# Kernel optimization log

Hardware: AMD Instinct MI355X
Metric: run time of the kernel (lower is better)

Reference implementation:

```python
import jax, jax.numpy as jnp
import numpy as np
from jax import lax

B, H, W, N = 4, 256, 256, 200000
DN = ('NHWC', 'HWIO', 'NHWC')


def _conv(x, w, padding):
    return lax.conv_general_dilated(x, w, (1, 1), padding, dimension_numbers=DN)


def _convT(x, w):
    # ConvTranspose2d(k=3, stride=2, padding=0): out = 2*H + 1
    return lax.conv_transpose(x, w, (2, 2), 'VALID', dimension_numbers=DN)


def setup_inputs() -> dict:
    key = jax.random.key(0)
    ks = jax.random.split(key, 12)
    features = jax.random.normal(ks[0], (N, 32), jnp.float32)
    bi = jax.random.randint(ks[1], (N, 1), 0, B)
    yi = jax.random.randint(ks[2], (N, 1), 0, H)
    xi = jax.random.randint(ks[3], (N, 1), 0, W)
    coors = jnp.concatenate([bi, yi, xi], axis=1).astype(jnp.int32)

    def p(k, shape):
        return jax.random.normal(k, shape, jnp.float32) * 0.05

    return dict(
        features=features, coors=coors, batch_size=B,
        w1=p(ks[4], (3, 3, 32, 64)), b1=p(ks[5], (64,)),
        w2=p(ks[6], (3, 3, 64, 64)), b2=p(ks[7], (64,)),
        w3=p(ks[8], (3, 3, 64, 64)), b3=p(ks[9], (64,)),
        wt=p(ks[10], (3, 3, 64, 64)), bt=p(ks[11], (64,)),
        w5=p(jax.random.fold_in(key, 99), (3, 3, 64, 64)),
        b5=p(jax.random.fold_in(key, 100), (64,)),
    )


def reference(features, coors, batch_size, w1, b1, w2, b2, w3, b3, wt, bt, w5, b5):
    bidx, yidx, xidx = coors[:, 0], coors[:, 1], coors[:, 2]
    # densify sparse voxels: [B,H,W,32]
    x = jnp.zeros((batch_size, H, W, 32), features.dtype).at[bidx, yidx, xidx].add(features)
    # active-site mask of the input sparse tensor
    mask0 = jnp.zeros((batch_size, H, W, 1), features.dtype).at[bidx, yidx, xidx, 0].set(1.0)
    ones3 = jnp.ones((3, 3, 1, 1), features.dtype)

    # SparseConv2d(32->64, k3, s1, p1): output active set = 3x3 dilation of input sites
    mask1 = (_conv(mask0, ones3, 'SAME') > 0).astype(features.dtype)
    h = jax.nn.relu((_conv(x, w1, 'SAME') + b1) * mask1)
    # two SubMConv2d(64,64,3): output restricted to the same active set
    h = jax.nn.relu((_conv(h, w2, 'SAME') + b2) * mask1)
    h = jax.nn.relu((_conv(h, w3, 'SAME') + b3) * mask1)
    # SparseConvTranspose2d(64,64,3,stride=2): active set = transpose-conv dilation
    mask4 = (_convT(mask1, ones3) > 0).astype(features.dtype)  # [B,2H+1,2W+1,1]
    h = jax.nn.relu((_convT(h, wt) + bt) * mask4)
    # ToDense already done implicitly (h is dense); final Conv2d(64,64,3) VALID + ReLU
    out = jax.nn.relu(_conv(h, w5, 'VALID') + b5)  # [B,2H-1,2W-1,64]
    return out
```

## Files before the change

kernel.cpp:

```cpp
#include <hip/hip_runtime.h>

#define BATCH 4
#define HH 256
#define WW 256
#define HT 513
#define HO 511

typedef __attribute__((ext_vector_type(8))) short bf16x8;
typedef __attribute__((ext_vector_type(4))) float f32x4;

__device__ __forceinline__ unsigned short f2bf(float f) {
    unsigned b = __float_as_uint(f);
    unsigned r = (b + 0x7fffu + ((b >> 16) & 1u)) >> 16;
    return (unsigned short)r;
}

typedef __attribute__((address_space(3))) unsigned int lds_u32;
typedef const __attribute__((address_space(1))) unsigned int g_u32;
__device__ __forceinline__ void gload16(const void* g, void* l) {
    __builtin_amdgcn_global_load_lds((g_u32*)g, (lds_u32*)l, 16, 0, 0);
}

__global__ void k_zero(float* __restrict__ p, int n4) {
    int i = blockIdx.x * blockDim.x + threadIdx.x;
    if (i < n4) ((float4*)p)[i] = make_float4(0.f, 0.f, 0.f, 0.f);
}

__global__ void k_scatter(const float* __restrict__ feat,
                          const int* __restrict__ coors,
                          float* __restrict__ x, float* __restrict__ mask0, int N) {
    int t = blockIdx.x * blockDim.x + threadIdx.x;
    int n = t >> 5, c = t & 31;
    if (n >= N) return;
    int b  = coors[n * 3 + 0];
    int y  = coors[n * 3 + 1];
    int xx = coors[n * 3 + 2];
    float f = feat[n * 32 + c];
    int pix = (b * HH + y) * WW + xx;
    atomicAdd(&x[pix * 32 + c], f);
    if (c == 0) mask0[pix] = 1.0f;
}

__global__ void k_mask1(const float* __restrict__ mask0, float* __restrict__ mask1, int total) {
    int t = blockIdx.x * blockDim.x + threadIdx.x;
    if (t >= total) return;
    int xx = t % WW;
    int y  = (t / WW) % HH;
    int b  = t / (WW * HH);
    float m = 0.f;
    #pragma unroll
    for (int dy = -1; dy <= 1; ++dy) {
        int iy = y + dy;
        if ((unsigned)iy >= HH) continue;
        #pragma unroll
        for (int dx = -1; dx <= 1; ++dx) {
            int ix = xx + dx;
            if ((unsigned)ix >= WW) continue;
            m = fmaxf(m, mask0[(b * HH + iy) * WW + ix]);
        }
    }
    mask1[t] = (m > 0.f) ? 1.f : 0.f;
}

__global__ void k_mask4(const float* __restrict__ mask1, float* __restrict__ mask4, int total) {
    int t = blockIdx.x * blockDim.x + threadIdx.x;
    if (t >= total) return;
    int ox = t % HT;
    int oy = (t / HT) % HT;
    int b  = t / (HT * HT);
    float m = 0.f;
    #pragma unroll
    for (int ky = 0; ky < 3; ++ky) {
        int q = oy + ky - 2;
        if ((q & 1) || (unsigned)(q >> 1) >= (unsigned)HH) continue;
        int iy = q >> 1;
        #pragma unroll
        for (int kx = 0; kx < 3; ++kx) {
            int r = ox + kx - 2;
            if ((r & 1) || (unsigned)(r >> 1) >= (unsigned)WW) continue;
            m = fmaxf(m, mask1[(b * HH + iy) * WW + (r >> 1)]);
        }
    }
    mask4[t] = (m > 0.f) ? 1.f : 0.f;
}

__global__ void k_cast(const float* __restrict__ src, unsigned short* __restrict__ dst, int n8) {
    int i = blockIdx.x * blockDim.x + threadIdx.x;
    if (i >= n8) return;
    float4 a = ((const float4*)src)[2 * i];
    float4 c = ((const float4*)src)[2 * i + 1];
    uint4 o;
    o.x = (unsigned)f2bf(a.x) | ((unsigned)f2bf(a.y) << 16);
    o.y = (unsigned)f2bf(a.z) | ((unsigned)f2bf(a.w) << 16);
    o.z = (unsigned)f2bf(c.x) | ((unsigned)f2bf(c.y) << 16);
    o.w = (unsigned)f2bf(c.z) | ((unsigned)f2bf(c.w) << 16);
    ((uint4*)dst)[i] = o;
}

__global__ void k_pack(const float* __restrict__ w, unsigned short* __restrict__ dst, int T) {
    int t = blockIdx.x * blockDim.x + threadIdx.x;
    if (t >= T * 256) return;
    int step = t >> 8;
    int r = t & 255;
    int nb = r >> 6;
    int l = r & 63;
    int k = step * 32 + ((l >> 4) * 8);
    int n = nb * 16 + (l & 15);
    unsigned short tmp[8];
    #pragma unroll
    for (int j = 0; j < 8; ++j) tmp[j] = f2bf(w[(size_t)(k + j) * 64 + n]);
    uint4 o;
    o.x = (unsigned)tmp[0] | ((unsigned)tmp[1] << 16);
    o.y = (unsigned)tmp[2] | ((unsigned)tmp[3] << 16);
    o.z = (unsigned)tmp[4] | ((unsigned)tmp[5] << 16);
    o.w = (unsigned)tmp[6] | ((unsigned)tmp[7] << 16);
    *(uint4*)(dst + (size_t)((step * 4 + nb) * 64 + l) * 8) = o;
}

template <int CIN, int IN_H, int IN_W, int OUT_H, int OUT_W, int PAD,
          bool MASKED, bool OUT_F32>
__global__ __launch_bounds__(512, 1) void k_conv2(
    const unsigned short* __restrict__ in,
    const unsigned short* __restrict__ bp,
    const float* __restrict__ bias,
    const float* __restrict__ mask,
    const unsigned short* __restrict__ zpg,
    void* __restrict__ outv)
{
    constexpr int H2  = CIN / 32;
    constexpr int XT  = (OUT_W + 255) / 256;
    constexpr int CPX = CIN / 8;
    constexpr int CSH = (CIN == 64) ? 3 : 2;
    constexpr int APX = (CIN == 32) ? 272 : 264;
    constexpr int ACH = APX * CPX;
    constexpr int ASZ = APX * CIN * 2;
    constexpr int BSZ = 3 * H2 * 4096;
    constexpr int BCH = 3 * H2 * 256;
    constexpr int PAIRS = (OUT_H + 1) / 2;

    extern __shared__ __align__(16) char lds[];

    int nwg  = (int)gridDim.x;
    int orig = (int)blockIdx.x;
    int q8 = nwg >> 3, r8 = nwg & 7;
    int xcd = orig & 7, pos = orig >> 3;
    int blk = (xcd < r8 ? xcd * (q8 + 1) : r8 * (q8 + 1) + (xcd - r8) * q8) + pos;

    int s  = blk % XT;
    int yp = (blk / XT) % PAIRS;
    int b  = blk / (XT * PAIRS);
    int y0 = yp * 2;

    int tid  = threadIdx.x;
    int lane = tid & 63;
    int wid  = tid >> 6;
    int r    = wid >> 2;
    int ww   = wid & 3;
    int m    = lane & 15;
    int quad = lane >> 4;

    int px_base = s * 256 + ww * 64;
    int pb = ww * 64 + m;
    int t0 = s * 256 - PAD;

    auto stageA = [&](int rel) {
        int iy = y0 - PAD + rel;
        bool rv = (unsigned)iy < (unsigned)IN_H;
        const unsigned short* inrow = in + (size_t)(b * IN_H + iy) * IN_W * CIN;
        char* base = lds + 2 * BSZ + (rel % 3) * ASZ;
        #pragma unroll
        for (int j = 0; j < (ACH + 511) / 512; ++j) {
            int ci = j * 512 + tid;
            if (ci >= ACH) break;
            int p  = ci >> CSH;
            int cc = ci & (CPX - 1);
            int swz = (CIN == 64) ? (p & 7) : ((p >> 1) & 3);
            int c  = cc ^ swz;
            int t  = t0 + p;
            const unsigned short* g = (rv && (unsigned)t < (unsigned)IN_W)
                ? inrow + (size_t)t * CIN + c * 8 : zpg;
            gload16(g, base + (size_t)(ci & ~63) * 16);
        }
    };
    auto stageB = [&](int ky) {
        const uint4* bsrc = (const uint4*)bp + (size_t)ky * BCH;
        char* base = lds + (ky & 1) * BSZ;
        #pragma unroll
        for (int j = 0; j < (BCH + 511) / 512; ++j) {
            int ci = j * 512 + tid;
            if (ci >= BCH) break;
            gload16(bsrc + ci, base + (size_t)(ci & ~63) * 16);
        }
    };

    f32x4 acc[4][4] = {};

    auto doKy = [&](int ky) {
        const unsigned short* lA_ =
            (const unsigned short*)(lds + 2 * BSZ + ((r + ky) % 3) * ASZ);
        const unsigned short* lB_ = (const unsigned short*)(lds + (ky & 1) * BSZ);
        #pragma unroll
        for (int kx = 0; kx < 3; ++kx) {
            #pragma unroll
            for (int half = 0; half < H2; ++half) {
                int tl = kx * H2 + half;
                const unsigned short* lbt = lB_ + tl * 2048 + lane * 8;
                bf16x8 bfr[4];
                #pragma unroll
                for (int nb = 0; nb < 4; ++nb)
                    bfr[nb] = *(const bf16x8*)(lbt + nb * 512);
                #pragma unroll
                for (int f = 0; f < 4; ++f) {
                    int p = pb + f * 16 + kx;
                    int swz = (CIN == 64) ? (p & 7) : ((p >> 1) & 3);
                    int c = ((CIN == 64) ? (half * 4 + quad) : quad) ^ swz;
                    bf16x8 a = *(const bf16x8*)(lA_ + (size_t)p * CIN + c * 8);
                    #pragma unroll
                    for (int nb = 0; nb < 4; ++nb)
                        acc[f][nb] = __builtin_amdgcn_mfma_f32_16x16x32_bf16(
                            a, bfr[nb], acc[f][nb], 0, 0, 0);
                }
            }
        }
    };

    stageA(0); stageA(1); stageA(2); stageB(0); stageB(1);
    __syncthreads();
    doKy(0);
    __syncthreads();
    stageA(3); stageB(2);
    doKy(1);
    __syncthreads();
    doKy(2);

    int y = y0 + r;
    if (y < OUT_H) {
        int n0 = m;
        float bv[4];
        #pragma unroll
        for (int nb = 0; nb < 4; ++nb) bv[nb] = bias[nb * 16 + n0];
        #pragma unroll
        for (int f = 0; f < 4; ++f) {
            #pragma unroll
            for (int reg = 0; reg < 4; ++reg) {
                int i = f * 16 + quad * 4 + reg;
                int pm = px_base + i;
                if (pm >= OUT_W) continue;
                size_t pix = (size_t)(b * OUT_H + y) * OUT_W + pm;
                float mk = 1.f;
                if constexpr (MASKED) mk = mask[pix];
                #pragma unroll
                for (int nb = 0; nb < 4; ++nb) {
                    float o = fmaxf((acc[f][nb][reg] + bv[nb]) * mk, 0.f);
                    if constexpr (OUT_F32)
                        ((float*)outv)[pix * 64 + nb * 16 + n0] = o;
                    else
                        ((unsigned short*)outv)[pix * 64 + nb * 16 + n0] = f2bf(o);
                }
            }
        }
    }
}

enum Mode { CONV, CONVT2 };

template <int CIN, int IN_H, int IN_W, int OUT_H, int OUT_W, int PAD,
          Mode MODE, bool MASKED, bool OUT_F32>
__global__ __launch_bounds__(256, 2) void k_conv_mfma(
    const unsigned short* __restrict__ in,
    const unsigned short* __restrict__ bp,
    const float* __restrict__ bias,
    const float* __restrict__ mask,
    const unsigned short* __restrict__ zpg,
    void* __restrict__ outv)
{
    constexpr int H2  = CIN / 32;
    constexpr int XT  = (OUT_W + 255) / 256;
    constexpr int CPX = CIN / 8;
    constexpr int CSH = (CIN == 64) ? 3 : 2;
    constexpr int APX = (MODE == CONV) ? ((CIN == 32) ? 320 : 288) : 160;
    constexpr int NITER = APX * CPX / 256;
    constexpr int BBYTES = 3 * H2 * 4096;

    __shared__ __align__(16) char lds[BBYTES + APX * CIN * 2];

    int nwg  = (int)gridDim.x;
    int orig = (int)blockIdx.x;
    int q8 = nwg >> 3, r8 = nwg & 7;
    int xcd = orig & 7, pos = orig >> 3;
    int blk = (xcd < r8 ? xcd * (q8 + 1) : r8 * (q8 + 1) + (xcd - r8) * q8) + pos;

    int s = blk % XT;
    int y = (blk / XT) % OUT_H;
    int b = blk / (XT * OUT_H);
    int tid  = threadIdx.x;
    int lane = tid & 63;
    int wid  = tid >> 6;
    int m    = lane & 15;
    int quad = lane >> 4;

    int px_base, par;
    if constexpr (MODE == CONV) { px_base = s * 256 + wid * 64; par = 0; }
    else { par = wid & 1; px_base = s * 256 + (wid >> 1) * 128; }

    int nkx, kx0, kxstep;
    if constexpr (MODE == CONV) { nkx = 3; kx0 = 0; kxstep = 1; }
    else { nkx = (par == 0) ? 2 : 1; kx0 = par; kxstep = 2; }

    int t0;
    if constexpr (MODE == CONV) t0 = s * 256 - PAD;
    else                        t0 = s * 128 - 1;

    int pb;
    if constexpr (MODE == CONV) pb = wid * 64 + m;
    else                        pb = (wid >> 1) * 64 + m;

    const unsigned short* lA = (const unsigned short*)(lds + BBYTES);
    const unsigned short* lB = (const unsigned short*)lds;

    f32x4 acc[4][4] = {};

    #pragma unroll
    for (int ky = 0; ky < 3; ++ky) {
        int iy; bool rowv;
        if constexpr (MODE == CONV) {
            iy = y + ky - PAD;
            rowv = (unsigned)iy < (unsigned)IN_H;
        } else {
            int q = y + ky - 2;
            rowv = (!(q & 1)) && ((unsigned)(q >> 1) < (unsigned)IN_H);
            iy = q >> 1;
        }
        if (!rowv) continue;

        const unsigned short* inrow = in + (size_t)(b * IN_H + iy) * IN_W * CIN;

        __syncthreads();
        {
            const uint4* bsrc = (const uint4*)bp + (size_t)ky * 3 * H2 * 256;
            #pragma unroll
            for (int j = 0; j < 3 * H2; ++j)
                gload16(bsrc + j * 256 + tid,
                        lds + (size_t)(j * 256 + (tid & ~63)) * 16);
        }
        #pragma unroll
        for (int j = 0; j < NITER; ++j) {
            int ci = j * 256 + tid;
            int p  = ci >> CSH;
            int cc = ci & (CPX - 1);
            int swz = (CIN == 64) ? (p & 7) : ((p >> 1) & 3);
            int c  = cc ^ swz;
            int t  = t0 + p;
            const unsigned short* g =
                ((unsigned)t < (unsigned)IN_W) ? inrow + (size_t)t * CIN + c * 8 : zpg;
            gload16(g, lds + BBYTES + (size_t)(j * 256 + (tid & ~63)) * 16);
        }
        __syncthreads();

        #pragma unroll
        for (int i = 0; i < 3; ++i) {
            if (i < nkx) {
                int kx = kx0 + i * kxstep;
                int kxo;
                if constexpr (MODE == CONV) kxo = kx;
                else kxo = ((par + kx - 2) >> 1) + 1;
                #pragma unroll
                for (int half = 0; half < H2; ++half) {
                    int tl = kx * H2 + half;
                    const unsigned short* lbt = lB + tl * 2048 + lane * 8;
                    bf16x8 bfr[4];
                    #pragma unroll
                    for (int nb = 0; nb < 4; ++nb)
                        bfr[nb] = *(const bf16x8*)(lbt + nb * 512);
                    #pragma unroll
                    for (int f = 0; f < 4; ++f) {
                        int p = pb + f * 16 + kxo;
                        int swz = (CIN == 64) ? (p & 7) : ((p >> 1) & 3);
                        int c = ((CIN == 64) ? (half * 4 + quad) : quad) ^ swz;
                        bf16x8 a = *(const bf16x8*)(lA + (size_t)p * CIN + c * 8);
                        #pragma unroll
                        for (int nb = 0; nb < 4; ++nb)
                            acc[f][nb] = __builtin_amdgcn_mfma_f32_16x16x32_bf16(
                                a, bfr[nb], acc[f][nb], 0, 0, 0);
                    }
                }
            }
        }
    }

    int n0 = m;
    float bv[4];
    #pragma unroll
    for (int nb = 0; nb < 4; ++nb) bv[nb] = bias[nb * 16 + n0];
    #pragma unroll
    for (int f = 0; f < 4; ++f) {
        #pragma unroll
        for (int reg = 0; reg < 4; ++reg) {
            int i = f * 16 + quad * 4 + reg;
            int pm;
            if constexpr (MODE == CONV) pm = px_base + i;
            else pm = px_base + 2 * i + par;
            if (pm >= OUT_W) continue;
            size_t pix = (size_t)(b * OUT_H + y) * OUT_W + pm;
            float mk = 1.f;
            if constexpr (MASKED) mk = mask[pix];
            #pragma unroll
            for (int nb = 0; nb < 4; ++nb) {
                float o = fmaxf((acc[f][nb][reg] + bv[nb]) * mk, 0.f);
                if constexpr (OUT_F32)
                    ((float*)outv)[pix * 64 + nb * 16 + n0] = o;
                else
                    ((unsigned short*)outv)[pix * 64 + nb * 16 + n0] = f2bf(o);
            }
        }
    }
}

extern "C" void kernel_launch(void* const* d_in, const int* in_sizes, int n_in,
                              void* d_out, int out_size, void* d_ws, size_t ws_size,
                              hipStream_t stream) {
    const float* feat = (const float*)d_in[0];
    const int* coors  = (const int*)d_in[1];
    const float* w1 = (const float*)d_in[3];
    const float* b1 = (const float*)d_in[4];
    const float* w2 = (const float*)d_in[5];
    const float* b2 = (const float*)d_in[6];
    const float* w3 = (const float*)d_in[7];
    const float* b3 = (const float*)d_in[8];
    const float* wt = (const float*)d_in[9];
    const float* bt = (const float*)d_in[10];
    const float* w5 = (const float*)d_in[11];
    const float* b5 = (const float*)d_in[12];

    int N = in_sizes[0] / 32;

    const size_t MB = 1024 * 1024;
    char* ws = (char*)d_ws;
    unsigned short* pk1 = (unsigned short*)(ws);
    unsigned short* pk2 = (unsigned short*)(ws + 36864);
    unsigned short* pk3 = (unsigned short*)(ws + 110592);
    unsigned short* pkt = (unsigned short*)(ws + 184320);
    unsigned short* pk5 = (unsigned short*)(ws + 258048);
    unsigned short* zpg = (unsigned short*)(ws + 960 * 1024);
    float* mask1 = (float*)(ws + 1 * MB);
    float* mask4 = (float*)(ws + 2 * MB);
    float* mask0 = (float*)(ws + 7 * MB);
    float* x_f32 = (float*)(ws + 8 * MB);
    unsigned short* x_bf  = (unsigned short*)(ws + 42 * MB);
    unsigned short* h1    = (unsigned short*)(ws + 59 * MB);
    unsigned short* h2    = (unsigned short*)(ws + 93 * MB);
    unsigned short* h3    = (unsigned short*)(ws + 8 * MB);
    unsigned short* h4    = (unsigned short*)(ws + 42 * MB);

    int nz4 = (262144 + 8388608) / 4;
    k_zero<<<(nz4 + 255) / 256, 256, 0, stream>>>(mask0, nz4);
    k_zero<<<1, 16, 0, stream>>>((float*)zpg, 16);

    k_scatter<<<(N * 32 + 255) / 256, 256, 0, stream>>>(feat, coors, x_f32, mask0, N);

    k_mask1<<<(BATCH * HH * WW) / 256, 256, 0, stream>>>(mask0, mask1, BATCH * HH * WW);
    int m4tot = BATCH * HT * HT;
    k_mask4<<<(m4tot + 255) / 256, 256, 0, stream>>>(mask1, mask4, m4tot);
    k_cast<<<(1048576 + 255) / 256, 256, 0, stream>>>(x_f32, x_bf, 1048576);
    k_pack<<<9, 256, 0, stream>>>(w1, pk1, 9);
    k_pack<<<18, 256, 0, stream>>>(w2, pk2, 18);
    k_pack<<<18, 256, 0, stream>>>(w3, pk3, 18);
    k_pack<<<18, 256, 0, stream>>>(wt, pkt, 18);
    k_pack<<<18, 256, 0, stream>>>(w5, pk5, 18);

    constexpr size_t LDS32 = 2 * 12288 + 3 * (272 * 32 * 2);
    constexpr size_t LDS64 = 2 * 24576 + 3 * (264 * 64 * 2);

    k_conv2<32, 256, 256, 256, 256, 1, true, false>
        <<<BATCH * 128 * 1, 512, LDS32, stream>>>(x_bf, pk1, b1, mask1, zpg, h1);
    k_conv2<64, 256, 256, 256, 256, 1, true, false>
        <<<BATCH * 128 * 1, 512, LDS64, stream>>>(h1, pk2, b2, mask1, zpg, h2);
    k_conv2<64, 256, 256, 256, 256, 1, true, false>
        <<<BATCH * 128 * 1, 512, LDS64, stream>>>(h2, pk3, b3, mask1, zpg, h3);

    k_conv_mfma<64, 256, 256, HT, HT, 0, CONVT2, true, false>
        <<<BATCH * HT * 3, 256, 0, stream>>>(h3, pkt, bt, mask4, zpg, h4);

    k_conv2<64, HT, HT, HO, HO, 0, false, true>
        <<<BATCH * 256 * 2, 512, LDS64, stream>>>(h4, pk5, b5, nullptr, zpg, (float*)d_out);
}
```

Before: 555.0 us.

## Restructure conv kernel to one output row per block with register A reuse

Replaces the two-row, 512-thread conv kernel with a 256-thread kernel that computes one output row per block and runs several blocks per CU. Each wave now owns 4 interleaved pixels per lane, so six A fragments loaded once into registers cover all three kx taps, which cuts LDS reads. Weights are read directly from global/L2 instead of being staged in LDS. Input rows are staged one ky at a time with syncs between them, and rows that fall into the padding are skipped. The cost is no overlap between load and compute within a block and three times more input-row staging per output row, which the higher occupancy is meant to hide.

```diff
diff --git a/kernel.cpp b/kernel.cpp
--- a/kernel.cpp
+++ b/kernel.cpp
@@ -119,7 +119,7 @@
 
 template <int CIN, int IN_H, int IN_W, int OUT_H, int OUT_W, int PAD,
           bool MASKED, bool OUT_F32>
-__global__ __launch_bounds__(512, 1) void k_conv2(
+__global__ __launch_bounds__(256, 3) void k_conv3(
     const unsigned short* __restrict__ in,
     const unsigned short* __restrict__ bp,
     const float* __restrict__ bias,
@@ -131,14 +131,11 @@
     constexpr int XT  = (OUT_W + 255) / 256;
     constexpr int CPX = CIN / 8;
     constexpr int CSH = (CIN == 64) ? 3 : 2;
-    constexpr int APX = (CIN == 32) ? 272 : 264;
+    constexpr int APX = (CIN == 32) ? 320 : 288;
     constexpr int ACH = APX * CPX;
-    constexpr int ASZ = APX * CIN * 2;
-    constexpr int BSZ = 3 * H2 * 4096;
-    constexpr int BCH = 3 * H2 * 256;
-    constexpr int PAIRS = (OUT_H + 1) / 2;
-
-    extern __shared__ __align__(16) char lds[];
+    constexpr int NITER = ACH / 256;
+
+    __shared__ __align__(16) char lds[APX * CIN * 2];
 
     int nwg  = (int)gridDim.x;
     int orig = (int)blockIdx.x;
@@ -146,117 +143,92 @@
     int xcd = orig & 7, pos = orig >> 3;
     int blk = (xcd < r8 ? xcd * (q8 + 1) : r8 * (q8 + 1) + (xcd - r8) * q8) + pos;
 
-    int s  = blk % XT;
-    int yp = (blk / XT) % PAIRS;
-    int b  = blk / (XT * PAIRS);
-    int y0 = yp * 2;
-
+    int s = blk % XT;
+    int y = (blk / XT) % OUT_H;
+    int b = blk / (XT * OUT_H);
     int tid  = threadIdx.x;
     int lane = tid & 63;
     int wid  = tid >> 6;
-    int r    = wid >> 2;
-    int ww   = wid & 3;
     int m    = lane & 15;
     int quad = lane >> 4;
 
-    int px_base = s * 256 + ww * 64;
-    int pb = ww * 64 + m;
-    int t0 = s * 256 - PAD;
-
-    auto stageA = [&](int rel) {
-        int iy = y0 - PAD + rel;
-        bool rv = (unsigned)iy < (unsigned)IN_H;
+    int P0    = s * 256 + wid * 64;
+    int pbase = wid * 64 + m * 4;
+    int t0    = s * 256 - PAD;
+
+    const uint4* bp4 = (const uint4*)bp;
+
+    f32x4 acc[4][4] = {};
+
+    #pragma unroll
+    for (int ky = 0; ky < 3; ++ky) {
+        int iy = y + ky - PAD;
+        if ((unsigned)iy >= (unsigned)IN_H) continue;
+
         const unsigned short* inrow = in + (size_t)(b * IN_H + iy) * IN_W * CIN;
-        char* base = lds + 2 * BSZ + (rel % 3) * ASZ;
-        #pragma unroll
-        for (int j = 0; j < (ACH + 511) / 512; ++j) {
-            int ci = j * 512 + tid;
-            if (ci >= ACH) break;
+
+        __syncthreads();
+        #pragma unroll
+        for (int j = 0; j < NITER; ++j) {
+            int ci = j * 256 + tid;
             int p  = ci >> CSH;
             int cc = ci & (CPX - 1);
-            int swz = (CIN == 64) ? (p & 7) : ((p >> 1) & 3);
-            int c  = cc ^ swz;
+            int c  = cc ^ ((p >> 2) & (CPX - 1));
             int t  = t0 + p;
-            const unsigned short* g = (rv && (unsigned)t < (unsigned)IN_W)
-                ? inrow + (size_t)t * CIN + c * 8 : zpg;
-            gload16(g, base + (size_t)(ci & ~63) * 16);
-        }
-    };
-    auto stageB = [&](int ky) {
-        const uint4* bsrc = (const uint4*)bp + (size_t)ky * BCH;
-        char* base = lds + (ky & 1) * BSZ;
-        #pragma unroll
-        for (int j = 0; j < (BCH + 511) / 512; ++j) {
-            int ci = j * 512 + tid;
-            if (ci >= BCH) break;
-            gload16(bsrc + ci, base + (size_t)(ci & ~63) * 16);
-        }
-    };
-
-    f32x4 acc[4][4] = {};
-
-    auto doKy = [&](int ky) {
-        const unsigned short* lA_ =
-            (const unsigned short*)(lds + 2 * BSZ + ((r + ky) % 3) * ASZ);
-        const unsigned short* lB_ = (const unsigned short*)(lds + (ky & 1) * BSZ);
-        #pragma unroll
-        for (int kx = 0; kx < 3; ++kx) {
+            const unsigned short* g =
+                ((unsigned)t < (unsigned)IN_W) ? inrow + (size_t)t * CIN + c * 8 : zpg;
+            gload16(g, lds + (size_t)(ci & ~63) * 16);
+        }
+        __syncthreads();
+
+        #pragma unroll
+        for (int half = 0; half < H2; ++half) {
+            int chq = (CIN == 64) ? (half * 4 + quad) : quad;
+            bf16x8 av[6];
             #pragma unroll
-            for (int half = 0; half < H2; ++half) {
-                int tl = kx * H2 + half;
-                const unsigned short* lbt = lB_ + tl * 2048 + lane * 8;
+            for (int v = 0; v < 6; ++v) {
+                int p = pbase + v;
+                int c = chq ^ ((p >> 2) & (CPX - 1));
+                av[v] = *(const bf16x8*)(lds + (size_t)p * (CIN * 2) + c * 16);
+            }
+            #pragma unroll
+            for (int kx = 0; kx < 3; ++kx) {
+                int t = (ky * 3 + kx) * H2 + half;
                 bf16x8 bfr[4];
                 #pragma unroll
                 for (int nb = 0; nb < 4; ++nb)
-                    bfr[nb] = *(const bf16x8*)(lbt + nb * 512);
+                    bfr[nb] = __builtin_bit_cast(bf16x8,
+                        bp4[(size_t)(t * 4 + nb) * 64 + lane]);
                 #pragma unroll
-                for (int f = 0; f < 4; ++f) {
-                    int p = pb + f * 16 + kx;
-                    int swz = (CIN == 64) ? (p & 7) : ((p >> 1) & 3);
-                    int c = ((CIN == 64) ? (half * 4 + quad) : quad) ^ swz;
-                    bf16x8 a = *(const bf16x8*)(lA_ + (size_t)p * CIN + c * 8);
+                for (int f = 0; f < 4; ++f)
                     #pragma unroll
                     for (int nb = 0; nb < 4; ++nb)
                         acc[f][nb] = __builtin_amdgcn_mfma_f32_16x16x32_bf16(
-                            a, bfr[nb], acc[f][nb], 0, 0, 0);
-                }
+                            av[f + kx], bfr[nb], acc[f][nb], 0, 0, 0);
             }
         }
-    };
-
-    stageA(0); stageA(1); stageA(2); stageB(0); stageB(1);
-    __syncthreads();
-    doKy(0);
-    __syncthreads();
-    stageA(3); stageB(2);
-    doKy(1);
-    __syncthreads();
-    doKy(2);
-
-    int y = y0 + r;
-    if (y < OUT_H) {
-        int n0 = m;
-        float bv[4];
-        #pragma unroll
-        for (int nb = 0; nb < 4; ++nb) bv[nb] = bias[nb * 16 + n0];
-        #pragma unroll
-        for (int f = 0; f < 4; ++f) {
+    }
+
+    int n0 = m;
+    float bv[4];
+    #pragma unroll
+    for (int nb = 0; nb < 4; ++nb) bv[nb] = bias[nb * 16 + n0];
+    #pragma unroll
+    for (int f = 0; f < 4; ++f) {
+        #pragma unroll
+        for (int reg = 0; reg < 4; ++reg) {
+            int pm = P0 + quad * 16 + reg * 4 + f;
+            if (pm >= OUT_W) continue;
+            size_t pix = (size_t)(b * OUT_H + y) * OUT_W + pm;
+            float mk = 1.f;
+            if constexpr (MASKED) mk = mask[pix];
             #pragma unroll
-            for (int reg = 0; reg < 4; ++reg) {
-                int i = f * 16 + quad * 4 + reg;
-                int pm = px_base + i;
-                if (pm >= OUT_W) continue;
-                size_t pix = (size_t)(b * OUT_H + y) * OUT_W + pm;
-                float mk = 1.f;
-                if constexpr (MASKED) mk = mask[pix];
-                #pragma unroll
-                for (int nb = 0; nb < 4; ++nb) {
-                    float o = fmaxf((acc[f][nb][reg] + bv[nb]) * mk, 0.f);
-                    if constexpr (OUT_F32)
-                        ((float*)outv)[pix * 64 + nb * 16 + n0] = o;
-                    else
-                        ((unsigned short*)outv)[pix * 64 + nb * 16 + n0] = f2bf(o);
-                }
+            for (int nb = 0; nb < 4; ++nb) {
+                float o = fmaxf((acc[f][nb][reg] + bv[nb]) * mk, 0.f);
+                if constexpr (OUT_F32)
+                    ((float*)outv)[pix * 64 + nb * 16 + n0] = o;
+                else
+                    ((unsigned short*)outv)[pix * 64 + nb * 16 + n0] = f2bf(o);
             }
         }
     }
@@ -468,19 +440,16 @@
     k_pack<<<18, 256, 0, stream>>>(wt, pkt, 18);
     k_pack<<<18, 256, 0, stream>>>(w5, pk5, 18);
 
-    constexpr size_t LDS32 = 2 * 12288 + 3 * (272 * 32 * 2);
-    constexpr size_t LDS64 = 2 * 24576 + 3 * (264 * 64 * 2);
-
-    k_conv2<32, 256, 256, 256, 256, 1, true, false>
-        <<<BATCH * 128 * 1, 512, LDS32, stream>>>(x_bf, pk1, b1, mask1, zpg, h1);
-    k_conv2<64, 256, 256, 256, 256, 1, true, false>
-        <<<BATCH * 128 * 1, 512, LDS64, stream>>>(h1, pk2, b2, mask1, zpg, h2);
-    k_conv2<64, 256, 256, 256, 256, 1, true, false>
-        <<<BATCH * 128 * 1, 512, LDS64, stream>>>(h2, pk3, b3, mask1, zpg, h3);
+    k_conv3<32, 256, 256, 256, 256, 1, true, false>
+        <<<BATCH * HH * 1, 256, 0, stream>>>(x_bf, pk1, b1, mask1, zpg, h1);
+    k_conv3<64, 256, 256, 256, 256, 1, true, false>
+        <<<BATCH * HH * 1, 256, 0, stream>>>(h1, pk2, b2, mask1, zpg, h2);
+    k_conv3<64, 256, 256, 256, 256, 1, true, false>
+        <<<BATCH * HH * 1, 256, 0, stream>>>(h2, pk3, b3, mask1, zpg, h3);
 
     k_conv_mfma<64, 256, 256, HT, HT, 0, CONVT2, true, false>
         <<<BATCH * HT * 3, 256, 0, stream>>>(h3, pkt, bt, mask4, zpg, h4);
 
-    k_conv2<64, HT, HT, HO, HO, 0, false, true>
-        <<<BATCH * 256 * 2, 512, LDS64, stream>>>(h4, pk5, b5, nullptr, zpg, (float*)d_out);
-}
+    k_conv3<64, HT, HT, HO, HO, 0, false, true>
+        <<<BATCH * HO * 2, 256, 0, stream>>>(h4, pk5, b5, nullptr, zpg, (float*)d_out);
+}
```

Result: slower. 570.6 us (+2.8%).
